# Performance work log

Hardware: AMD Instinct MI355X
Metric: run time of the kernel (lower is better)

## Reference

```python
import jax, jax.numpy as jnp
import numpy as np

N_NODES = 100000
N_EDGES = 3200000
N_FEAT = 16
HID = 64
DEPTH = 4
N_GRAPHS = 1000


def setup_inputs() -> dict:
    key = jax.random.key(0)
    ks = jax.random.split(key, 12)
    x = jax.random.normal(ks[0], (N_NODES, N_FEAT), dtype=jnp.float32)
    edge_index = jax.random.randint(ks[1], (2, N_EDGES), 0, N_NODES, dtype=jnp.int32)
    edge_attr = jax.random.normal(ks[2], (N_EDGES, 4), dtype=jnp.float32)
    batch = jnp.sort(jax.random.randint(ks[3], (N_NODES,), 0, N_GRAPHS, dtype=jnp.int32))
    # GCN layer params (Glorot-ish scaling)
    Wi = jax.random.normal(ks[4], (N_FEAT, HID), dtype=jnp.float32) / np.sqrt(N_FEAT)
    bi = jnp.zeros((HID,), dtype=jnp.float32)
    Wh = jax.random.normal(ks[5], (DEPTH, HID, HID), dtype=jnp.float32) / np.sqrt(HID)
    bh = jnp.zeros((DEPTH, HID), dtype=jnp.float32)
    # decoder MLP: hiddens -> hiddens//2 -> 4
    Wd1 = jax.random.normal(ks[6], (HID, HID // 2), dtype=jnp.float32) / np.sqrt(HID)
    bd1 = jnp.zeros((HID // 2,), dtype=jnp.float32)
    Wd2 = jax.random.normal(ks[7], (HID // 2, 4), dtype=jnp.float32) / np.sqrt(HID // 2)
    bd2 = jnp.zeros((4,), dtype=jnp.float32)
    return {"x": x, "edge_index": edge_index, "edge_attr": edge_attr, "batch": batch,
            "Wi": Wi, "bi": bi, "Wh": Wh, "bh": bh,
            "Wd1": Wd1, "bd1": bd1, "Wd2": Wd2, "bd2": bd2}


def _gcn_conv(h, src, dst, norm, W, b, n_nodes):
    # GCNConv: out = scatter_add(norm * (X W)[src] -> dst) + b  (self-loops already in src/dst)
    hW = h @ W                              # [N, out]
    msg = hW[src] * norm[:, None]           # gather + normalize, [E+N, out]
    out = jax.ops.segment_sum(msg, dst, num_segments=n_nodes)
    return out + b


def reference(x, edge_index, edge_attr, batch, Wi, bi, Wh, bh, Wd1, bd1, Wd2, bd2):
    n = x.shape[0]
    loop = jnp.arange(n, dtype=edge_index.dtype)
    src = jnp.concatenate([edge_index[0], loop])   # add self-loops
    dst = jnp.concatenate([edge_index[1], loop])
    # symmetric normalization deg^{-1/2}[src] * deg^{-1/2}[dst]
    deg = jnp.zeros((n,), dtype=x.dtype).at[dst].add(1.0)
    dinv = jnp.where(deg > 0, jax.lax.rsqrt(deg), 0.0)
    norm = dinv[src] * dinv[dst]                   # [E+N]

    h = jax.nn.relu(_gcn_conv(x, src, dst, norm, Wi, bi, n))
    for i in range(Wh.shape[0]):
        h = jax.nn.relu(_gcn_conv(h, src, dst, norm, Wh[i], bh[i], n))

    z = jax.ops.segment_max(h, batch, num_segments=N_GRAPHS)   # global max pool [G, HID]
    probs = jax.nn.relu(z @ Wd1 + bd1) @ Wd2 + bd2             # [G, 4]
    return (probs, edge_attr)
```

## Files before the change

### kernel.cpp

```cpp
#include <hip/hip_runtime.h>
#include <math.h>


#define RBITS 9
#define RNODES (1 << RBITS)
#define PACK_SHIFT 23
#define SEGCAP 17408
#define PART_C 8192

typedef unsigned int uint32;
typedef _Float16 f16x2 __attribute__((ext_vector_type(2)));
typedef _Float16 f16x8 __attribute__((ext_vector_type(8)));
typedef float f32x2 __attribute__((ext_vector_type(2)));
typedef float f32x4 __attribute__((ext_vector_type(4)));

__device__ __forceinline__ uint32 h2_pack(float a, float b) {
  f16x2 t;
  t[0] = (_Float16)a;
  t[1] = (_Float16)b;
  return __builtin_bit_cast(uint32, t);
}

__device__ __forceinline__ uint32 fp8_rnd2(float a, float b) {
  a = fminf(fmaxf(a, -448.f), 448.f) * 0.00390625f;
  b = fminf(fmaxf(b, -448.f), 448.f) * 0.00390625f;
  uint32 ha = (uint32)__builtin_bit_cast(unsigned short, (_Float16)a);
  uint32 hb = (uint32)__builtin_bit_cast(unsigned short, (_Float16)b);
  uint32 ma = ((ha & 0x7FFFu) + 0x3Fu + ((ha >> 7) & 1u)) >> 7;
  uint32 mb = ((hb & 0x7FFFu) + 0x3Fu + ((hb >> 7) & 1u)) >> 7;
  ma = ma > 0x7Eu ? 0x7Eu : ma;
  mb = mb > 0x7Eu ? 0x7Eu : mb;
  return (((ha >> 8) & 0x80u) | ma) | (((((hb >> 8) & 0x80u) | mb)) << 8);
}

#if __has_builtin(__builtin_amdgcn_cvt_pk_f32_fp8)
#define FP8_PK_LO(u) __builtin_amdgcn_cvt_pk_f32_fp8((int)(u), false)
#define FP8_PK_HI(u) __builtin_amdgcn_cvt_pk_f32_fp8((int)(u), true)
#else
__device__ __forceinline__ f32x2 fp8_pk_sw(uint32 u) {
  uint32 t0 = (u & 0xFFu) | ((u & 0xFF00u) << 8);
  uint32 w = ((t0 & 0x00800080u) << 8) | ((t0 & 0x007F007Fu) << 7);
  f16x2 h = __builtin_bit_cast(f16x2, w);
  f32x2 r;
  r.x = (float)h[0] * 256.f;
  r.y = (float)h[1] * 256.f;
  return r;
}
#define FP8_PK_LO(u) fp8_pk_sw(u)
#define FP8_PK_HI(u) fp8_pk_sw((u) >> 16)
#endif

__global__ void init_bcur_kernel(int* __restrict__ bcur, int nbuck) {
  int b = blockIdx.x * blockDim.x + threadIdx.x;
  if (b < nbuck) bcur[b] = b * SEGCAP;
}

__global__ __launch_bounds__(512) void partition_sort_kernel(const int* __restrict__ src,
                                                             const int* __restrict__ dst,
                                                             int* __restrict__ bcur,
                                                             int* __restrict__ part, int e,
                                                             int nbuck) {
  __shared__ int hist[256];
  __shared__ int loff[256];
  __shared__ int gbase[256];
  __shared__ int tmp[256];
  __shared__ int sval[PART_C];
  int tid = threadIdx.x;
  int s = blockIdx.x * PART_C;
  int cnt = min(e - s, PART_C);
  if (tid < 256) hist[tid] = 0;
  __syncthreads();
  for (int i = tid; i < cnt; i += 512)
    atomicAdd(&hist[((uint32)dst[s + i]) >> RBITS], 1);
  __syncthreads();
  if (tid < 256) tmp[tid] = hist[tid];
  __syncthreads();
  for (int st = 1; st < 256; st <<= 1) {
    int v = 0;
    if (tid < 256 && tid >= st) v = tmp[tid - st];
    __syncthreads();
    if (tid < 256) tmp[tid] += v;
    __syncthreads();
  }
  if (tid < 256) {
    loff[tid] = tmp[tid] - hist[tid];
    int c = hist[tid];
    gbase[tid] = (tid < nbuck && c > 0) ? atomicAdd(&bcur[tid], c) : 0;
    hist[tid] = 0;
  }
  __syncthreads();
  for (int i = tid; i < cnt; i += 512) {
    int d = dst[s + i];
    int b = ((uint32)d) >> RBITS;
    int pos = loff[b] + atomicAdd(&hist[b], 1);
    sval[pos] = src[s + i] | ((d & (RNODES - 1)) << PACK_SHIFT);
  }
  __syncthreads();
  int wave = tid >> 6, lane = tid & 63;
  for (int b = wave; b < nbuck; b += 8) {
    int c = hist[b];
    int g = gbase[b], lo = loff[b];
    int lim = (b + 1) * SEGCAP - g;
    if (c > lim) c = lim;
    for (int j = lane; j < c; j += 64) part[g + j] = sval[lo + j];
  }
}

__global__ __launch_bounds__(1024) void bucket_fill_kernel(const int* __restrict__ part,
                                                           const int* __restrict__ bcur,
                                                           int* __restrict__ spad,
                                                           int* __restrict__ counts, int n,
                                                           int cap) {
  __shared__ int cur[RNODES];
  int b = blockIdx.x;
  for (int t = threadIdx.x; t < RNODES; t += 1024) cur[t] = 0;
  __syncthreads();
  int s = b * SEGCAP;
  int en = min(bcur[b], s + SEGCAP);
  int lo = b << RBITS;
  for (int i = s + threadIdx.x; i < en; i += 1024) {
    int e = part[i];
    int srcv = e & ((1 << PACK_SHIFT) - 1);
    int local = ((uint32)e) >> PACK_SHIFT;
    int p = atomicAdd(&cur[local], 1);
    if (p < cap) spad[(size_t)(lo + local) * cap + p] = srcv;
  }
  __syncthreads();
  for (int t = threadIdx.x; t < RNODES; t += 1024) {
    int v = lo + t;
    if (v < n) counts[v] = cur[t];
  }
}

__global__ __launch_bounds__(256) void dinv_kernel(const int* __restrict__ counts,
                                                   float* __restrict__ dinv, int n) {
  int i = blockIdx.x * blockDim.x + threadIdx.x;
  if (i < n) dinv[i] = rsqrtf((float)(counts[i] + 1));
}

__global__ __launch_bounds__(256) void scale_x_kernel(const float4* __restrict__ x4,
                                                      const float* __restrict__ dinv,
                                                      uint4* __restrict__ gx4, int n) {
  int v = blockIdx.x * blockDim.x + threadIdx.x;
  if (v >= n) return;
  float d = dinv[v];
  uint32 o[4];
#pragma unroll
  for (int q = 0; q < 4; ++q) {
    float4 xv = x4[(size_t)v * 4 + q];
    o[q] = fp8_rnd2(d * xv.x, d * xv.y) | (fp8_rnd2(d * xv.z, d * xv.w) << 16);
  }
  gx4[v] = make_uint4(o[0], o[1], o[2], o[3]);
}

__global__ __launch_bounds__(256) void agg16_kernel(const uint32* __restrict__ gx,
                                                    const int* __restrict__ spad,
                                                    const int* __restrict__ counts,
                                                    const float* __restrict__ dinv,
                                                    uint2* __restrict__ xa2, int n, int cap) {
  int wave = (int)((blockIdx.x * blockDim.x + threadIdx.x) >> 6);
  int lane = threadIdx.x & 63;
  int grp = lane >> 2, p = lane & 3;
  int v = wave * 16 + grp;
  bool valid = v < n;
  int vc = valid ? v : (n - 1);
  int cnt = valid ? min(counts[vc], cap) : 0;
  const int* eb = spad + (size_t)vc * cap;
  f32x2 a0[2], a1[2], a2[2], a3[2];
#pragma unroll
  for (int j = 0; j < 2; ++j) { a0[j] = 0.f; a1[j] = 0.f; a2[j] = 0.f; a3[j] = 0.f; }
  if (valid) {
    uint32 z = gx[(size_t)vc * 4 + p];
    a0[0] = FP8_PK_LO(z);
    a0[1] = FP8_PK_HI(z);
  }
#define ACC2(acc, gw)                \
  {                                  \
    uint32 zz = (gw);                \
    (acc)[0] += FP8_PK_LO(zz);       \
    (acc)[1] += FP8_PK_HI(zz);       \
  }
  int quads = cnt >> 2, rem = cnt & 3;
  if (quads > 0) {
    const int4* eb4 = (const int4*)eb;
    int4 idx = eb4[0];
    for (int q = 1; q < quads; ++q) {
      int4 nxt = eb4[q];
      ACC2(a0, gx[(size_t)idx.x * 4 + p])
      ACC2(a1, gx[(size_t)idx.y * 4 + p])
      ACC2(a2, gx[(size_t)idx.z * 4 + p])
      ACC2(a3, gx[(size_t)idx.w * 4 + p])
      idx = nxt;
    }
    ACC2(a0, gx[(size_t)idx.x * 4 + p])
    ACC2(a1, gx[(size_t)idx.y * 4 + p])
    ACC2(a2, gx[(size_t)idx.z * 4 + p])
    ACC2(a3, gx[(size_t)idx.w * 4 + p])
  }
  int tb = quads << 2;
  for (int r = 0; r < rem; ++r) ACC2(a0, gx[(size_t)eb[tb + r] * 4 + p])
#undef ACC2
#pragma unroll
  for (int j = 0; j < 2; ++j) a0[j] = (a0[j] + a1[j]) + (a2[j] + a3[j]);
  if (valid) {
    float d = dinv[vc];
    uint2 o;
    o.x = h2_pack(d * a0[0].x, d * a0[0].y);
    o.y = h2_pack(d * a0[1].x, d * a0[1].y);
    xa2[(size_t)vc * 4 + p] = o;
  }
}

__global__ __launch_bounds__(256) void matmul16_mfma_kernel(const uint4* __restrict__ xa4,
                                                            const float* __restrict__ Wi,
                                                            const float* __restrict__ bi,
                                                            uint32* __restrict__ h32, int n,
                                                            int ntiles) {
  int lane = threadIdx.x & 63;
  int col = lane & 15, grp = lane >> 4;
  f16x8 bhi[4], blo[4];
#pragma unroll
  for (int nn = 0; nn < 4; ++nn) {
    f16x8 hi = {0, 0, 0, 0, 0, 0, 0, 0}, lo = {0, 0, 0, 0, 0, 0, 0, 0};
    if (grp < 2) {
#pragma unroll
      for (int j = 0; j < 8; ++j) {
        float wv = Wi[(grp * 8 + j) * 64 + nn * 16 + col];
        _Float16 hb = (_Float16)wv;
        hi[j] = hb;
        lo[j] = (_Float16)(wv - (float)hb);
      }
    }
    bhi[nn] = hi;
    blo[nn] = lo;
  }
  float bv[4];
#pragma unroll
  for (int nn = 0; nn < 4; ++nn) bv[nn] = bi[nn * 16 + col];

  int wave = (int)((blockIdx.x * blockDim.x + threadIdx.x) >> 6);
  int nw = (int)((gridDim.x * blockDim.x) >> 6);
  for (int t = wave; t < ntiles; t += nw) {
    int vb = t * 16;
    int vA = min(vb + col, n - 1);
    f16x8 a = {0, 0, 0, 0, 0, 0, 0, 0};
    if (grp < 2) a = __builtin_bit_cast(f16x8, xa4[(size_t)vA * 2 + grp]);
    f32x4 acc[4];
#pragma unroll
    for (int nn = 0; nn < 4; ++nn) {
      f32x4 c = {0.f, 0.f, 0.f, 0.f};
      c = __builtin_amdgcn_mfma_f32_16x16x32_f16(a, bhi[nn], c, 0, 0, 0);
      c = __builtin_amdgcn_mfma_f32_16x16x32_f16(a, blo[nn], c, 0, 0, 0);
      acc[nn] = c;
    }
#pragma unroll
    for (int nn = 0; nn < 4; ++nn) {
#pragma unroll
      for (int r = 0; r < 4; ++r) {
        int vr = vb + grp * 4 + r;
        float val = fmaxf(acc[nn][r] + bv[nn], 0.f);
        float other = __shfl_xor(val, 1);
        if (!(col & 1) && vr < n)
          h32[(size_t)vr * 32 + ((nn * 16 + col) >> 1)] = h2_pack(val, other);
      }
    }
  }
}

__global__ __launch_bounds__(256) void matmul64_mfma_kernel(const uint4* __restrict__ h4,
                                                            const float* __restrict__ W,
                                                            const float* __restrict__ dinv,
                                                            unsigned short* __restrict__ g16,
                                                            int n, int ntiles) {
  int lane = threadIdx.x & 63;
  int col = lane & 15, grp = lane >> 4;
  f16x8 bhi[2][4], blo[2][4];
#pragma unroll
  for (int kk = 0; kk < 2; ++kk) {
#pragma unroll
    for (int nn = 0; nn < 4; ++nn) {
      f16x8 hi, lo;
#pragma unroll
      for (int j = 0; j < 8; ++j) {
        float wv = W[(kk * 32 + grp * 8 + j) * 64 + nn * 16 + col];
        _Float16 hb = (_Float16)wv;
        hi[j] = hb;
        lo[j] = (_Float16)(wv - (float)hb);
      }
      bhi[kk][nn] = hi;
      blo[kk][nn] = lo;
    }
  }
  int wave = (int)((blockIdx.x * blockDim.x + threadIdx.x) >> 6);
  int nw = (int)((gridDim.x * blockDim.x) >> 6);
  for (int t = wave; t < ntiles; t += nw) {
    int vb = t * 16;
    int vA = min(vb + col, n - 1);
    f16x8 a0 = __builtin_bit_cast(f16x8, h4[(size_t)vA * 8 + grp]);
    f16x8 a1 = __builtin_bit_cast(f16x8, h4[(size_t)vA * 8 + 4 + grp]);
    f32x4 acc[4];
#pragma unroll
    for (int nn = 0; nn < 4; ++nn) {
      f32x4 c = {0.f, 0.f, 0.f, 0.f};
      c = __builtin_amdgcn_mfma_f32_16x16x32_f16(a0, bhi[0][nn], c, 0, 0, 0);
      c = __builtin_amdgcn_mfma_f32_16x16x32_f16(a0, blo[0][nn], c, 0, 0, 0);
      c = __builtin_amdgcn_mfma_f32_16x16x32_f16(a1, bhi[1][nn], c, 0, 0, 0);
      c = __builtin_amdgcn_mfma_f32_16x16x32_f16(a1, blo[1][nn], c, 0, 0, 0);
      acc[nn] = c;
    }
    float dv[4];
#pragma unroll
    for (int r = 0; r < 4; ++r) dv[r] = dinv[min(vb + grp * 4 + r, n - 1)];
#pragma unroll
    for (int nn = 0; nn < 4; ++nn) {
#pragma unroll
      for (int r = 0; r < 4; ++r) {
        int vr = vb + grp * 4 + r;
        float val = acc[nn][r] * dv[r];
        float other = __shfl_xor(val, 1);
        if (!(col & 1) && vr < n)
          g16[(size_t)vr * 32 + ((nn * 16 + col) >> 1)] =
              (unsigned short)fp8_rnd2(val, other);
      }
    }
  }
}

__global__ __launch_bounds__(256) void agg64_kernel(const uint2* __restrict__ g2,
                                                    const int* __restrict__ spad,
                                                    const int* __restrict__ counts,
                                                    const float* __restrict__ dinv,
                                                    const float* __restrict__ bias,
                                                    uint4* __restrict__ hout4, int n, int cap) {
  int wave = (int)((blockIdx.x * blockDim.x + threadIdx.x) >> 6);
  int lane = threadIdx.x & 63;
  int grp = lane >> 3, p = lane & 7;
  int v = wave * 8 + grp;
  bool valid = v < n;
  int vc = valid ? v : (n - 1);
  int cnt = valid ? min(counts[vc], cap) : 0;
  const int* eb = spad + (size_t)vc * cap;
  f32x2 a0[4], a1[4], a2[4], a3[4];
#pragma unroll
  for (int j = 0; j < 4; ++j) { a0[j] = 0.f; a1[j] = 0.f; a2[j] = 0.f; a3[j] = 0.f; }
  if (valid) {
    uint2 s = g2[(size_t)vc * 8 + p];
    a0[0] = FP8_PK_LO(s.x);
    a0[1] = FP8_PK_HI(s.x);
    a0[2] = FP8_PK_LO(s.y);
    a0[3] = FP8_PK_HI(s.y);
  }
#define ACCD(acc, dd)                \
  {                                  \
    uint2 zz = (dd);                 \
    (acc)[0] += FP8_PK_LO(zz.x);     \
    (acc)[1] += FP8_PK_HI(zz.x);     \
    (acc)[2] += FP8_PK_LO(zz.y);     \
    (acc)[3] += FP8_PK_HI(zz.y);     \
  }
  int octs = cnt >> 3, rem = cnt & 7;
  const int4* eb4 = (const int4*)eb;
  for (int q = 0; q < octs; ++q) {
    int4 i0 = eb4[2 * q];
    int4 i1 = eb4[2 * q + 1];
    uint2 d0 = g2[(size_t)i0.x * 8 + p];
    uint2 d1 = g2[(size_t)i0.y * 8 + p];
    uint2 d2 = g2[(size_t)i0.z * 8 + p];
    uint2 d3 = g2[(size_t)i0.w * 8 + p];
    uint2 d4 = g2[(size_t)i1.x * 8 + p];
    uint2 d5 = g2[(size_t)i1.y * 8 + p];
    uint2 d6 = g2[(size_t)i1.z * 8 + p];
    uint2 d7 = g2[(size_t)i1.w * 8 + p];
    ACCD(a0, d0) ACCD(a1, d1) ACCD(a2, d2) ACCD(a3, d3)
    ACCD(a0, d4) ACCD(a1, d5) ACCD(a2, d6) ACCD(a3, d7)
  }
  int tb = octs << 3;
  for (int r = 0; r < rem; ++r) {
    uint2 d = g2[(size_t)eb[tb + r] * 8 + p];
    ACCD(a0, d)
  }
#undef ACCD
#pragma unroll
  for (int j = 0; j < 4; ++j) a0[j] = (a0[j] + a1[j]) + (a2[j] + a3[j]);
  if (valid) {
    float d = dinv[vc];
    float4 b0 = ((const float4*)bias)[2 * p];
    float4 b1 = ((const float4*)bias)[2 * p + 1];
    uint4 o;
    o.x = h2_pack(fmaxf(fmaf(d, a0[0].x, b0.x), 0.f),
                  fmaxf(fmaf(d, a0[0].y, b0.y), 0.f));
    o.y = h2_pack(fmaxf(fmaf(d, a0[1].x, b0.z), 0.f),
                  fmaxf(fmaf(d, a0[1].y, b0.w), 0.f));
    o.z = h2_pack(fmaxf(fmaf(d, a0[2].x, b1.x), 0.f),
                  fmaxf(fmaf(d, a0[2].y, b1.y), 0.f));
    o.w = h2_pack(fmaxf(fmaf(d, a0[3].x, b1.z), 0.f),
                  fmaxf(fmaf(d, a0[3].y, b1.w), 0.f));
    hout4[(size_t)vc * 8 + p] = o;
  }
}

__global__ __launch_bounds__(256) void graph_starts_kernel(const int* __restrict__ batch,
                                                           int* __restrict__ starts, int n,
                                                           int ngr) {
  int i = blockIdx.x * blockDim.x + threadIdx.x;
  if (i >= n) return;
  int b = batch[i];
  int bp = (i == 0) ? -1 : batch[i - 1];
  for (int gg = bp + 1; gg <= b; ++gg) starts[gg] = i;
  if (i == n - 1)
    for (int gg = b + 1; gg <= ngr; ++gg) starts[gg] = n;
}

__global__ __launch_bounds__(64) void pool_max_kernel(const uint32* __restrict__ h32,
                                                      const int* __restrict__ starts,
                                                      float* __restrict__ z, int ngr) {
  int gI = blockIdx.x;
  if (gI >= ngr) return;
  int lane = threadIdx.x;
  int s = starts[gI], e = starts[gI + 1];
  float m = -INFINITY;
  for (int i = s; i < e; ++i) {
    uint32 w = h32[(size_t)i * 32 + (lane >> 1)];
    f16x2 t = __builtin_bit_cast(f16x2, w);
    m = fmaxf(m, (float)t[lane & 1]);
  }
  z[(size_t)gI * 64 + lane] = m;
}

__global__ __launch_bounds__(64) void decoder_kernel(const float* __restrict__ z,
                                                     const float* __restrict__ Wd1,
                                                     const float* __restrict__ bd1,
                                                     const float* __restrict__ Wd2,
                                                     const float* __restrict__ bd2,
                                                     float* __restrict__ probs, int ngr) {
  __shared__ float zs[64];
  __shared__ float hs[32];
  int gI = blockIdx.x;
  if (gI >= ngr) return;
  int t = threadIdx.x;
  zs[t] = z[(size_t)gI * 64 + t];
  __syncthreads();
  if (t < 32) {
    float acc = bd1[t];
#pragma unroll
    for (int k = 0; k < 64; ++k) acc = fmaf(zs[k], Wd1[k * 32 + t], acc);
    hs[t] = fmaxf(acc, 0.f);
  }
  __syncthreads();
  if (t < 4) {
    float acc = bd2[t];
#pragma unroll
    for (int k = 0; k < 32; ++k) acc = fmaf(hs[k], Wd2[k * 4 + t], acc);
    probs[(size_t)gI * 4 + t] = acc;
  }
}

__global__ __launch_bounds__(256) void copy4_kernel(const float4* __restrict__ in,
                                                    float4* __restrict__ out, int n4) {
  int stride = gridDim.x * blockDim.x;
  for (int i = blockIdx.x * blockDim.x + threadIdx.x; i < n4; i += stride) out[i] = in[i];
}

extern "C" void kernel_launch(void* const* d_in, const int* in_sizes, int n_in,
                              void* d_out, int out_size, void* d_ws, size_t ws_size,
                              hipStream_t stream) {
  const float* x  = (const float*)d_in[0];
  const int* ei   = (const int*)d_in[1];
  const float* ea = (const float*)d_in[2];
  const int* batch = (const int*)d_in[3];
  const float* Wi = (const float*)d_in[4];
  const float* bi = (const float*)d_in[5];
  const float* Wh = (const float*)d_in[6];
  const float* bh = (const float*)d_in[7];
  const float* Wd1 = (const float*)d_in[8];
  const float* bd1 = (const float*)d_in[9];
  const float* Wd2 = (const float*)d_in[10];
  const float* bd2 = (const float*)d_in[11];

  const int N = in_sizes[3];
  const int E = in_sizes[1] / 2;
  const int DEPTH = in_sizes[6] / (64 * 64);
  const int G = (out_size - E * 4) / 4;
  const int* srcIdx = ei;
  const int* dstIdx = ei + E;
  const int NTILES = (N + 15) / 16;
  const int NBUCK = (N + RNODES - 1) >> RBITS;

  auto rup = [](size_t b) { return (b + 255) & ~(size_t)255; };
  size_t fixed_bytes = rup((size_t)N * 4) + rup((size_t)N * 4) +
                       rup((size_t)N * 64) + rup((size_t)N * 128) +
                       rup((size_t)N * 32) +
                       rup((size_t)(G + 1) * 4) + rup((size_t)G * 64 * 4) +
                       rup((size_t)NBUCK * 4) + 8192;
  int CAP = 96;
  while (CAP > 64 && fixed_bytes + rup((size_t)N * CAP * 4) > ws_size) CAP -= 16;

  char* w = (char*)d_ws;
  auto alloc = [&](size_t bytes) {
    void* p = (void*)w;
    w += (bytes + 255) & ~(size_t)255;
    return p;
  };
  int* counts   = (int*)alloc((size_t)N * 4);
  float* dinv   = (float*)alloc((size_t)N * 4);
  void* gbuf    = alloc((size_t)N * 64);
  uint32* hbuf  = (uint32*)alloc((size_t)N * 128);
  uint32* xabuf = (uint32*)alloc((size_t)N * 32);
  int* starts   = (int*)alloc((size_t)(G + 1) * 4);
  float* zbuf   = (float*)alloc((size_t)G * 64 * 4);
  int* bcur     = (int*)alloc((size_t)NBUCK * 4);
  int* spad     = (int*)alloc((size_t)N * CAP * 4);
  int* part     = (int*)hbuf;
  (void)ws_size; (void)n_in;

  float* probs_out = (float*)d_out;
  float* ea_out    = (float*)d_out + (size_t)G * 4;

  const int NBP = (E + PART_C - 1) / PART_C;
  init_bcur_kernel<<<(NBUCK + 255) / 256, 256, 0, stream>>>(bcur, NBUCK);
  partition_sort_kernel<<<NBP, 512, 0, stream>>>(srcIdx, dstIdx, bcur, part, E, NBUCK);
  bucket_fill_kernel<<<NBUCK, 1024, 0, stream>>>(part, bcur, spad, counts, N, CAP);
  dinv_kernel<<<(N + 255) / 256, 256, 0, stream>>>(counts, dinv, N);

  scale_x_kernel<<<(N + 255) / 256, 256, 0, stream>>>((const float4*)x, dinv,
                                                      (uint4*)gbuf, N);
  agg16_kernel<<<(N + 63) / 64, 256, 0, stream>>>((const uint32*)gbuf, spad, counts, dinv,
                                                  (uint2*)xabuf, N, CAP);
  matmul16_mfma_kernel<<<512, 256, 0, stream>>>((const uint4*)xabuf, Wi, bi, hbuf, N, NTILES);

  for (int l = 0; l < DEPTH; ++l) {
    matmul64_mfma_kernel<<<512, 256, 0, stream>>>((const uint4*)hbuf,
                                                  Wh + (size_t)l * 64 * 64, dinv,
                                                  (unsigned short*)gbuf, N, NTILES);
    agg64_kernel<<<(N + 31) / 32, 256, 0, stream>>>((const uint2*)gbuf, spad, counts, dinv,
                                                    bh + (size_t)l * 64, (uint4*)hbuf, N, CAP);
  }

  graph_starts_kernel<<<(N + 255) / 256, 256, 0, stream>>>(batch, starts, N, G);
  pool_max_kernel<<<G, 64, 0, stream>>>(hbuf, starts, zbuf, G);
  decoder_kernel<<<G, 64, 0, stream>>>(zbuf, Wd1, bd1, Wd2, bd2, probs_out, G);

  copy4_kernel<<<2048, 256, 0, stream>>>((const float4*)ea, (float4*)ea_out, E);
}
```

Before: 387.5 us.

## Stage per-node adjacency in LDS and sort neighbor lists before writing padded rows

Halves the destination bucket size, doubles the partition chunk and widens the histogram/scan to 512 entries. The bucket fill now builds each node's neighbor list in shared memory, insertion-sorts it by source index, and writes the padded adjacency rows to global memory as coalesced stores. Sorted sources should give more locality in the later gather passes, and coalesced stores replace scattered ones. In exchange it adds a serial per-thread sort, uses a large LDS footprint (about 100KB), and changes counts to be clamped at cap.

```diff
diff --git a/kernel.cpp b/kernel.cpp
--- a/kernel.cpp
+++ b/kernel.cpp
@@ -2,11 +2,12 @@
 #include <math.h>
 
 
-#define RBITS 9
+#define RBITS 8
 #define RNODES (1 << RBITS)
-#define PACK_SHIFT 23
-#define SEGCAP 17408
-#define PART_C 8192
+#define PACK_SHIFT 24
+#define SEGCAP 9216
+#define PART_C 16384
+#define CAP_L 97
 
 typedef unsigned int uint32;
 typedef _Float16 f16x2 __attribute__((ext_vector_type(2)));
@@ -60,29 +61,28 @@
                                                              int* __restrict__ bcur,
                                                              int* __restrict__ part, int e,
                                                              int nbuck) {
-  __shared__ int hist[256];
-  __shared__ int loff[256];
-  __shared__ int gbase[256];
-  __shared__ int tmp[256];
+  __shared__ int hist[512];
+  __shared__ int loff[512];
+  __shared__ int gbase[512];
+  __shared__ int tmp[512];
   __shared__ int sval[PART_C];
   int tid = threadIdx.x;
   int s = blockIdx.x * PART_C;
   int cnt = min(e - s, PART_C);
-  if (tid < 256) hist[tid] = 0;
+  hist[tid] = 0;
   __syncthreads();
   for (int i = tid; i < cnt; i += 512)
     atomicAdd(&hist[((uint32)dst[s + i]) >> RBITS], 1);
   __syncthreads();
-  if (tid < 256) tmp[tid] = hist[tid];
-  __syncthreads();
-  for (int st = 1; st < 256; st <<= 1) {
-    int v = 0;
-    if (tid < 256 && tid >= st) v = tmp[tid - st];
+  tmp[tid] = hist[tid];
+  __syncthreads();
+  for (int st = 1; st < 512; st <<= 1) {
+    int v = (tid >= st) ? tmp[tid - st] : 0;
     __syncthreads();
-    if (tid < 256) tmp[tid] += v;
+    tmp[tid] += v;
     __syncthreads();
   }
-  if (tid < 256) {
+  {
     loff[tid] = tmp[tid] - hist[tid];
     int c = hist[tid];
     gbase[tid] = (tid < nbuck && c > 0) ? atomicAdd(&bcur[tid], c) : 0;
@@ -112,23 +112,44 @@
                                                            int* __restrict__ counts, int n,
                                                            int cap) {
   __shared__ int cur[RNODES];
+  __shared__ int lists[RNODES * CAP_L];
   int b = blockIdx.x;
-  for (int t = threadIdx.x; t < RNODES; t += 1024) cur[t] = 0;
+  int tid = threadIdx.x;
+  for (int t = tid; t < RNODES; t += 1024) cur[t] = 0;
   __syncthreads();
   int s = b * SEGCAP;
   int en = min(bcur[b], s + SEGCAP);
-  int lo = b << RBITS;
-  for (int i = s + threadIdx.x; i < en; i += 1024) {
+  for (int i = s + tid; i < en; i += 1024) {
     int e = part[i];
     int srcv = e & ((1 << PACK_SHIFT) - 1);
     int local = ((uint32)e) >> PACK_SHIFT;
     int p = atomicAdd(&cur[local], 1);
-    if (p < cap) spad[(size_t)(lo + local) * cap + p] = srcv;
-  }
-  __syncthreads();
-  for (int t = threadIdx.x; t < RNODES; t += 1024) {
+    if (p < cap) lists[local * CAP_L + p] = srcv;
+  }
+  __syncthreads();
+  if (tid < RNODES) {
+    int c = min(cur[tid], cap);
+    int* L = &lists[tid * CAP_L];
+    for (int i = 1; i < c; ++i) {
+      int key = L[i];
+      int j = i - 1;
+      while (j >= 0 && L[j] > key) {
+        L[j + 1] = L[j];
+        --j;
+      }
+      L[j + 1] = key;
+    }
+  }
+  __syncthreads();
+  int lo = b << RBITS;
+  for (int idx = tid; idx < RNODES * cap; idx += 1024) {
+    int v = idx / cap, j = idx - v * cap;
+    if (lo + v < n && j < min(cur[v], cap))
+      spad[(size_t)(lo + v) * cap + j] = lists[v * CAP_L + j];
+  }
+  for (int t = tid; t < RNODES; t += 1024) {
     int v = lo + t;
-    if (v < n) counts[v] = cur[t];
+    if (v < n) counts[v] = min(cur[t], cap);
   }
 }
 
```

New measurement: 583.0 us. 50.5% more time.

## Split 64-wide fp8 features into two 32-wide planes and aggregate per plane

Applied to the files above, without the earlier changes.

The hidden-layer matmul now writes its fp8 output as two separate planes of 32 features each, instead of one interleaved 64-feature row per node. Aggregation runs as two passes, one per plane, with 4 lanes per node instead of 8. Each pass writes its half of the f16 output row with the matching half of the bias. The aim is to shrink the randomly gathered working set per pass so it stays in cache longer. In exchange, the neighbour index lists are read twice per layer and there is an extra kernel launch per layer.

```diff
diff --git a/kernel.cpp b/kernel.cpp
--- a/kernel.cpp
+++ b/kernel.cpp
@@ -291,6 +291,7 @@
       blo[kk][nn] = lo;
     }
   }
+  size_t plane_stride = (size_t)n * 16;
   int wave = (int)((blockIdx.x * blockDim.x + threadIdx.x) >> 6);
   int nw = (int)((gridDim.x * blockDim.x) >> 6);
   for (int t = wave; t < ntiles; t += nw) {
@@ -319,23 +320,24 @@
         float val = acc[nn][r] * dv[r];
         float other = __shfl_xor(val, 1);
         if (!(col & 1) && vr < n)
-          g16[(size_t)vr * 32 + ((nn * 16 + col) >> 1)] =
-              (unsigned short)fp8_rnd2(val, other);
+          g16[(size_t)(nn >> 1) * plane_stride + (size_t)vr * 16 +
+              (((nn & 1) * 16 + col) >> 1)] = (unsigned short)fp8_rnd2(val, other);
       }
     }
   }
 }
 
-__global__ __launch_bounds__(256) void agg64_kernel(const uint2* __restrict__ g2,
-                                                    const int* __restrict__ spad,
-                                                    const int* __restrict__ counts,
-                                                    const float* __restrict__ dinv,
-                                                    const float* __restrict__ bias,
-                                                    uint4* __restrict__ hout4, int n, int cap) {
+__global__ __launch_bounds__(256) void agg64_pass_kernel(const uint2* __restrict__ gp,
+                                                         const int* __restrict__ spad,
+                                                         const int* __restrict__ counts,
+                                                         const float* __restrict__ dinv,
+                                                         const float* __restrict__ bias32,
+                                                         uint4* __restrict__ hout4, int n,
+                                                         int cap, int half) {
   int wave = (int)((blockIdx.x * blockDim.x + threadIdx.x) >> 6);
   int lane = threadIdx.x & 63;
-  int grp = lane >> 3, p = lane & 7;
-  int v = wave * 8 + grp;
+  int grp = lane >> 2, p = lane & 3;
+  int v = wave * 16 + grp;
   bool valid = v < n;
   int vc = valid ? v : (n - 1);
   int cnt = valid ? min(counts[vc], cap) : 0;
@@ -344,7 +346,7 @@
 #pragma unroll
   for (int j = 0; j < 4; ++j) { a0[j] = 0.f; a1[j] = 0.f; a2[j] = 0.f; a3[j] = 0.f; }
   if (valid) {
-    uint2 s = g2[(size_t)vc * 8 + p];
+    uint2 s = gp[(size_t)vc * 4 + p];
     a0[0] = FP8_PK_LO(s.x);
     a0[1] = FP8_PK_HI(s.x);
     a0[2] = FP8_PK_LO(s.y);
@@ -363,20 +365,20 @@
   for (int q = 0; q < octs; ++q) {
     int4 i0 = eb4[2 * q];
     int4 i1 = eb4[2 * q + 1];
-    uint2 d0 = g2[(size_t)i0.x * 8 + p];
-    uint2 d1 = g2[(size_t)i0.y * 8 + p];
-    uint2 d2 = g2[(size_t)i0.z * 8 + p];
-    uint2 d3 = g2[(size_t)i0.w * 8 + p];
-    uint2 d4 = g2[(size_t)i1.x * 8 + p];
-    uint2 d5 = g2[(size_t)i1.y * 8 + p];
-    uint2 d6 = g2[(size_t)i1.z * 8 + p];
-    uint2 d7 = g2[(size_t)i1.w * 8 + p];
+    uint2 d0 = gp[(size_t)i0.x * 4 + p];
+    uint2 d1 = gp[(size_t)i0.y * 4 + p];
+    uint2 d2 = gp[(size_t)i0.z * 4 + p];
+    uint2 d3 = gp[(size_t)i0.w * 4 + p];
+    uint2 d4 = gp[(size_t)i1.x * 4 + p];
+    uint2 d5 = gp[(size_t)i1.y * 4 + p];
+    uint2 d6 = gp[(size_t)i1.z * 4 + p];
+    uint2 d7 = gp[(size_t)i1.w * 4 + p];
     ACCD(a0, d0) ACCD(a1, d1) ACCD(a2, d2) ACCD(a3, d3)
     ACCD(a0, d4) ACCD(a1, d5) ACCD(a2, d6) ACCD(a3, d7)
   }
   int tb = octs << 3;
   for (int r = 0; r < rem; ++r) {
-    uint2 d = g2[(size_t)eb[tb + r] * 8 + p];
+    uint2 d = gp[(size_t)eb[tb + r] * 4 + p];
     ACCD(a0, d)
   }
 #undef ACCD
@@ -384,8 +386,8 @@
   for (int j = 0; j < 4; ++j) a0[j] = (a0[j] + a1[j]) + (a2[j] + a3[j]);
   if (valid) {
     float d = dinv[vc];
-    float4 b0 = ((const float4*)bias)[2 * p];
-    float4 b1 = ((const float4*)bias)[2 * p + 1];
+    float4 b0 = ((const float4*)bias32)[2 * p];
+    float4 b1 = ((const float4*)bias32)[2 * p + 1];
     uint4 o;
     o.x = h2_pack(fmaxf(fmaf(d, a0[0].x, b0.x), 0.f),
                   fmaxf(fmaf(d, a0[0].y, b0.y), 0.f));
@@ -395,7 +397,7 @@
                   fmaxf(fmaf(d, a0[2].y, b1.y), 0.f));
     o.w = h2_pack(fmaxf(fmaf(d, a0[3].x, b1.z), 0.f),
                   fmaxf(fmaf(d, a0[3].y, b1.w), 0.f));
-    hout4[(size_t)vc * 8 + p] = o;
+    hout4[(size_t)vc * 8 + half * 4 + p] = o;
   }
 }
 
@@ -528,12 +530,18 @@
                                                   (uint2*)xabuf, N, CAP);
   matmul16_mfma_kernel<<<512, 256, 0, stream>>>((const uint4*)xabuf, Wi, bi, hbuf, N, NTILES);
 
+  const uint2* plane0 = (const uint2*)gbuf;
+  const uint2* plane1 = (const uint2*)((char*)gbuf + (size_t)N * 32);
   for (int l = 0; l < DEPTH; ++l) {
     matmul64_mfma_kernel<<<512, 256, 0, stream>>>((const uint4*)hbuf,
                                                   Wh + (size_t)l * 64 * 64, dinv,
                                                   (unsigned short*)gbuf, N, NTILES);
-    agg64_kernel<<<(N + 31) / 32, 256, 0, stream>>>((const uint2*)gbuf, spad, counts, dinv,
-                                                    bh + (size_t)l * 64, (uint4*)hbuf, N, CAP);
+    agg64_pass_kernel<<<(N + 63) / 64, 256, 0, stream>>>(plane0, spad, counts, dinv,
+                                                         bh + (size_t)l * 64, (uint4*)hbuf,
+                                                         N, CAP, 0);
+    agg64_pass_kernel<<<(N + 63) / 64, 256, 0, stream>>>(plane1, spad, counts, dinv,
+                                                         bh + (size_t)l * 64 + 32,
+                                                         (uint4*)hbuf, N, CAP, 1);
   }
 
   graph_starts_kernel<<<(N + 255) / 256, 256, 0, stream>>>(batch, starts, N, G);
```

After: 462.6 us. 19.4% more time.
